# Kernel tuning notes

Hardware: AMD Instinct MI355X
Metric: run time of the kernel (lower is better)

Reference implementation:

```python
import jax, jax.numpy as jnp
import numpy as np

DIM = 1024
HEADS = 16
HEAD_DIM = DIM // HEADS
HIDDEN = 4 * DIM
EPS = 1e-5

def _layernorm(x, w, b):
    mu = jnp.mean(x, axis=-1, keepdims=True)
    var = jnp.mean(jnp.square(x - mu), axis=-1, keepdims=True)
    return (x - mu) * jax.lax.rsqrt(var + EPS) * w + b

def setup_inputs() -> dict:
    key = jax.random.key(0)
    ks = jax.random.split(key, 8)
    B, N, C = 4, 1024, DIM
    s = lambda fan_in: 1.0 / np.sqrt(fan_in)
    return {
        "x": jax.random.normal(ks[0], (B, N, C), dtype=jnp.float32),
        "ln1_w": jnp.ones((C,), jnp.float32),
        "ln1_b": jnp.zeros((C,), jnp.float32),
        "qkv_w": jax.random.normal(ks[1], (3 * C, C), jnp.float32) * s(C),
        "proj_w": jax.random.normal(ks[2], (C, C), jnp.float32) * s(C),
        "proj_b": jnp.zeros((C,), jnp.float32),
        "ln2_w": jnp.ones((C,), jnp.float32),
        "ln2_b": jnp.zeros((C,), jnp.float32),
        "fc1_w": jax.random.normal(ks[3], (HIDDEN, C), jnp.float32) * s(C),
        "fc1_b": jnp.zeros((HIDDEN,), jnp.float32),
        "fc2_w": jax.random.normal(ks[4], (C, HIDDEN), jnp.float32) * s(HIDDEN),
        "fc2_b": jnp.zeros((C,), jnp.float32),
    }

def reference(x, ln1_w, ln1_b, qkv_w, proj_w, proj_b, ln2_w, ln2_b, fc1_w, fc1_b, fc2_w, fc2_b):
    B, N, C = x.shape
    H, D = HEADS, HEAD_DIM
    scale = D ** -0.5
    # --- attention branch (pre-norm) ---
    h = _layernorm(x, ln1_w, ln1_b)
    qkv = jnp.einsum('bnc,oc->bno', h, qkv_w)          # [B,N,3C], no bias (qkv_bias=False)
    qkv = qkv.reshape(B, N, 3, H, D)
    q = jnp.transpose(qkv[:, :, 0], (0, 2, 1, 3))       # [B,H,N,D]
    k = jnp.transpose(qkv[:, :, 1], (0, 2, 1, 3))
    v = jnp.transpose(qkv[:, :, 2], (0, 2, 1, 3))
    attn = jnp.einsum('bhnd,bhmd->bhnm', q, k) * scale  # [B,H,N,N]
    attn = jax.nn.softmax(attn, axis=-1)
    o = jnp.einsum('bhnm,bhmd->bhnd', attn, v)          # [B,H,N,D]
    o = jnp.transpose(o, (0, 2, 1, 3)).reshape(B, N, C)
    o = jnp.einsum('bnc,oc->bno', o, proj_w) + proj_b
    x = x + o
    # --- MLP branch (pre-norm); drop=0.0 -> identity ---
    h = _layernorm(x, ln2_w, ln2_b)
    h = jnp.einsum('bnc,hc->bnh', h, fc1_w) + fc1_b
    h = jax.nn.gelu(h, approximate=False)               # nn.GELU exact erf form
    h = jnp.einsum('bnh,ch->bnc', h, fc2_w) + fc2_b
    return x + h
```

## Files before the change

kernel.cpp:

```cpp
#include <hip/hip_runtime.h>
#include <hip/hip_bf16.h>
#include <math.h>
#include <stdint.h>

#define SEQ 1024
#define CDIM 1024
#define NHEAD 16
#define HIDDEN 4096
#define BATCH 4
#define MROWS (BATCH*SEQ)

using bf16x8 = __attribute__((ext_vector_type(8))) short;
using f32x4  = __attribute__((ext_vector_type(4))) float;

__device__ __forceinline__ short f2bf(float f) {
    union { float f; uint32_t u; } c; c.f = f;
    const uint32_t u = c.u + 0x7FFFu + ((c.u >> 16) & 1u);
    return (short)(u >> 16);
}

__device__ __forceinline__ float gelu_exact(float v) {
    return 0.5f * v * (1.0f + erff(v * 0.70710678118654752440f));
}

__device__ __forceinline__ void gload_lds16(const short* g, short* lds) {
    __builtin_amdgcn_global_load_lds(
        (const __attribute__((address_space(1))) void*)(uintptr_t)g,
        (__attribute__((address_space(3))) void*)(uintptr_t)lds,
        16, 0, 0);
}

__global__ void cvt_all_kernel(const float* __restrict__ qkv_w, const float* __restrict__ proj_w,
                               const float* __restrict__ fc1_w, const float* __restrict__ fc2_w,
                               short* __restrict__ wq, short* __restrict__ wp,
                               short* __restrict__ w1, short* __restrict__ w2) {
    const int blk = blockIdx.x;
    const float* in; short* out; size_t base;
    if (blk < 1536)      { in = qkv_w;  out = wq; base = (size_t)blk * 2048; }
    else if (blk < 2048) { in = proj_w; out = wp; base = (size_t)(blk - 1536) * 2048; }
    else if (blk < 4096) { in = fc1_w;  out = w1; base = (size_t)(blk - 2048) * 2048; }
    else                 { in = fc2_w;  out = w2; base = (size_t)(blk - 4096) * 2048; }
    const size_t i = base + (size_t)threadIdx.x * 8;
    const float4 a = *(const float4*)(in + i);
    const float4 b = *(const float4*)(in + i + 4);
    bf16x8 s;
    s[0] = f2bf(a.x); s[1] = f2bf(a.y); s[2] = f2bf(a.z); s[3] = f2bf(a.w);
    s[4] = f2bf(b.x); s[5] = f2bf(b.y); s[6] = f2bf(b.z); s[7] = f2bf(b.w);
    *(bf16x8*)(out + i) = s;
}

__global__ void ln_kernel(const float* __restrict__ x, const float* __restrict__ w,
                          const float* __restrict__ b, short* __restrict__ out) {
    const int row = blockIdx.x;
    const int t = threadIdx.x;
    const float4* xr = (const float4*)(x + (size_t)row * CDIM);
    float4 v = xr[t];
    float s  = v.x + v.y + v.z + v.w;
    float sq = v.x*v.x + v.y*v.y + v.z*v.z + v.w*v.w;
    #pragma unroll
    for (int off = 32; off; off >>= 1) {
        s  += __shfl_down(s, off);
        sq += __shfl_down(sq, off);
    }
    __shared__ float ss[4], ssq[4];
    const int wid = t >> 6, lane = t & 63;
    if (lane == 0) { ss[wid] = s; ssq[wid] = sq; }
    __syncthreads();
    s  = ss[0] + ss[1] + ss[2] + ss[3];
    sq = ssq[0] + ssq[1] + ssq[2] + ssq[3];
    const float mu  = s * (1.0f / CDIM);
    const float var = sq * (1.0f / CDIM) - mu * mu;
    const float rs  = rsqrtf(var + 1e-5f);
    const float4 wv = ((const float4*)w)[t];
    const float4 bv = ((const float4*)b)[t];
    short4 o;
    o.x = f2bf((v.x - mu) * rs * wv.x + bv.x);
    o.y = f2bf((v.y - mu) * rs * wv.y + bv.y);
    o.z = f2bf((v.z - mu) * rs * wv.z + bv.z);
    o.w = f2bf((v.w - mu) * rs * wv.w + bv.w);
    *(short4*)(out + (size_t)row * CDIM + t * 4) = o;
}

template<int BM, int BN, bool BIAS, bool RES, bool GELU_, bool OUTBF16>
__global__ __launch_bounds__(256) void mgemm(
    const short* __restrict__ A, const short* __restrict__ B,
    const float* __restrict__ bias, const float* __restrict__ res,
    void* __restrict__ Cv, int M, int N, int K)
{
    constexpr int MF = BM / 32;
    constexpr int NF = BN / 32;
    constexpr int CA = BM / 64;
    constexpr int CB = BN / 64;
    __shared__ __align__(16) short As[3][BM * 32];
    __shared__ __align__(16) short Bs[3][BN * 32];
    const int t = threadIdx.x;
    const int w = t >> 6, l = t & 63;

    const int gx = gridDim.x;
    const int nwg = gx * gridDim.y;
    const int lid = blockIdx.y * gx + blockIdx.x;
    const int swzb = (lid & 7) * (nwg >> 3) + (lid >> 3);
    const int bx = swzb % gx, by = swzb / gx;
    const int m0 = by * BM, n0 = bx * BN;

    const int wrow = (w >> 1) * (BM / 2);
    const int wcol = (w & 1) * (BN / 2);

    const int sk8 = ((l & 3) ^ ((l >> 3) & 3)) * 8;
    const short* agp = A + (size_t)(m0 + w * 16 * CA + (l >> 2)) * K + sk8;
    const short* bgp = B + (size_t)(n0 + w * 16 * CB + (l >> 2)) * K + sk8;

    const int fr = l & 15;
    const int rk = ((l >> 4) ^ ((fr >> 1) & 3)) * 8;
    int aoff[MF], boff[NF];
    #pragma unroll
    for (int m = 0; m < MF; ++m) aoff[m] = (wrow + m * 16 + fr) * 32 + rk;
    #pragma unroll
    for (int n = 0; n < NF; ++n) boff[n] = (wcol + n * 16 + fr) * 32 + rk;

    auto stage = [&](int k0, int buf) {
        #pragma unroll
        for (int c = 0; c < CA; ++c)
            gload_lds16(agp + (size_t)(c * 16) * K + k0, &As[buf][(w * CA + c) * 512]);
        #pragma unroll
        for (int c = 0; c < CB; ++c)
            gload_lds16(bgp + (size_t)(c * 16) * K + k0, &Bs[buf][(w * CB + c) * 512]);
    };

    f32x4 acc[MF][NF] = {};
    const int T = K / 32;
    stage(0, 0);
    stage(32, 1);
    int cur = 0;
    for (int kt = 0; kt < T; ++kt) {
        if (kt < T - 1) {
            if constexpr (CA + CB == 4) asm volatile("s_waitcnt vmcnt(4)" ::: "memory");
            else                        asm volatile("s_waitcnt vmcnt(3)" ::: "memory");
        } else {
            asm volatile("s_waitcnt vmcnt(0)" ::: "memory");
        }
        __builtin_amdgcn_s_barrier();
        if (kt + 2 < T) {
            int nb = kt + 2; nb -= (nb >= 3) ? ((nb / 3) * 3) : 0;
            stage((kt + 2) * 32, nb);
        }
        bf16x8 af[MF], bfr[NF];
        #pragma unroll
        for (int m = 0; m < MF; ++m) af[m]  = *(const bf16x8*)&As[cur][aoff[m]];
        #pragma unroll
        for (int n = 0; n < NF; ++n) bfr[n] = *(const bf16x8*)&Bs[cur][boff[n]];
        #pragma unroll
        for (int m = 0; m < MF; ++m)
            #pragma unroll
            for (int n = 0; n < NF; ++n)
                acc[m][n] = __builtin_amdgcn_mfma_f32_16x16x32_bf16(af[m], bfr[n], acc[m][n], 0, 0, 0);
        cur = (cur == 2) ? 0 : cur + 1;
    }

    const int lr4 = (l >> 4) * 4, lc = l & 15;
    #pragma unroll
    for (int m = 0; m < MF; ++m) {
        #pragma unroll
        for (int n = 0; n < NF; ++n) {
            const int col = n0 + wcol + n * 16 + lc;
            const float bv = BIAS ? bias[col] : 0.0f;
            #pragma unroll
            for (int r = 0; r < 4; ++r) {
                const int row = m0 + wrow + m * 16 + lr4 + r;
                float v = acc[m][n][r] + bv;
                if (GELU_) v = gelu_exact(v);
                if (RES)   v += res[(size_t)row * N + col];
                if (OUTBF16) ((short*)Cv)[(size_t)row * N + col] = f2bf(v);
                else         ((float*)Cv)[(size_t)row * N + col] = v;
            }
        }
    }
}

__global__ __launch_bounds__(256) void qkv_m(
    const short* __restrict__ A, const short* __restrict__ B,
    short* __restrict__ qkvb, short* __restrict__ VT, int K)
{
    __shared__ __align__(16) short As[3][128 * 32];
    __shared__ __align__(16) short Bs[3][128 * 32];
    const int t = threadIdx.x;
    const int w = t >> 6, l = t & 63;

    const int gx = gridDim.x;
    const int nwg = gx * gridDim.y;
    const int lid = blockIdx.y * gx + blockIdx.x;
    const int swzb = (lid & 7) * (nwg >> 3) + (lid >> 3);
    const int bx = swzb % gx, by = swzb / gx;
    const int m0 = by * 128, n0 = bx * 128;

    const int wrow = (w >> 1) * 64;
    const int wcol = (w & 1) * 64;

    const int sk8 = ((l & 3) ^ ((l >> 3) & 3)) * 8;
    const short* agp = A + (size_t)(m0 + w * 32 + (l >> 2)) * K + sk8;
    const short* bgp = B + (size_t)(n0 + w * 32 + (l >> 2)) * K + sk8;

    const int fr = l & 15;
    const int rk = ((l >> 4) ^ ((fr >> 1) & 3)) * 8;
    int aoff[4], boff[4];
    #pragma unroll
    for (int m = 0; m < 4; ++m) aoff[m] = (wrow + m * 16 + fr) * 32 + rk;
    #pragma unroll
    for (int n = 0; n < 4; ++n) boff[n] = (wcol + n * 16 + fr) * 32 + rk;

    auto stage = [&](int k0, int buf) {
        #pragma unroll
        for (int c = 0; c < 2; ++c)
            gload_lds16(agp + (size_t)(c * 16) * K + k0, &As[buf][(w * 2 + c) * 512]);
        #pragma unroll
        for (int c = 0; c < 2; ++c)
            gload_lds16(bgp + (size_t)(c * 16) * K + k0, &Bs[buf][(w * 2 + c) * 512]);
    };

    f32x4 acc[4][4] = {};
    const int T = K / 32;
    stage(0, 0);
    stage(32, 1);
    int cur = 0;
    for (int kt = 0; kt < T; ++kt) {
        if (kt < T - 1) asm volatile("s_waitcnt vmcnt(4)" ::: "memory");
        else            asm volatile("s_waitcnt vmcnt(0)" ::: "memory");
        __builtin_amdgcn_s_barrier();
        if (kt + 2 < T) {
            int nb = kt + 2; nb -= (nb >= 3) ? ((nb / 3) * 3) : 0;
            stage((kt + 2) * 32, nb);
        }
        bf16x8 af[4], bfr[4];
        #pragma unroll
        for (int m = 0; m < 4; ++m) af[m]  = *(const bf16x8*)&As[cur][aoff[m]];
        #pragma unroll
        for (int n = 0; n < 4; ++n) bfr[n] = *(const bf16x8*)&Bs[cur][boff[n]];
        #pragma unroll
        for (int m = 0; m < 4; ++m)
            #pragma unroll
            for (int n = 0; n < 4; ++n)
                acc[m][n] = __builtin_amdgcn_mfma_f32_16x16x32_bf16(af[m], bfr[n], acc[m][n], 0, 0, 0);
        cur = (cur == 2) ? 0 : cur + 1;
    }

    const int lr4 = (l >> 4) * 4, lc = l & 15;
    if (n0 < 2048) {
        const float sc = (n0 < 1024) ? 0.125f : 1.0f;
        #pragma unroll
        for (int m = 0; m < 4; ++m) {
            #pragma unroll
            for (int n = 0; n < 4; ++n) {
                const int col = n0 + wcol + n * 16 + lc;
                #pragma unroll
                for (int r = 0; r < 4; ++r) {
                    const int row = m0 + wrow + m * 16 + lr4 + r;
                    qkvb[(size_t)row * 2048 + col] = f2bf(acc[m][n][r] * sc);
                }
            }
        }
    } else {
        #pragma unroll
        for (int m = 0; m < 4; ++m) {
            const int row0 = m0 + wrow + m * 16 + lr4;
            const int b = row0 >> 10, nseq = row0 & 1023;
            #pragma unroll
            for (int n = 0; n < 4; ++n) {
                const int c2 = n0 - 2048 + wcol + n * 16 + lc;
                const int h = c2 >> 6, d = c2 & 63;
                short4 v4;
                v4.x = f2bf(acc[m][n][0]); v4.y = f2bf(acc[m][n][1]);
                v4.z = f2bf(acc[m][n][2]); v4.w = f2bf(acc[m][n][3]);
                *(short4*)&VT[(((size_t)(b * 16 + h) * 64 + d) * 1024) + nseq] = v4;
            }
        }
    }
}

__global__ __launch_bounds__(512) void fattn(const short* __restrict__ qkvb,
                                             const short* __restrict__ VT,
                                             short* __restrict__ o) {
    const int lid = blockIdx.y * gridDim.x + blockIdx.x;
    const int bh = ((lid >> 6) << 3) | (lid & 7);
    const int q0 = ((lid >> 3) & 7) * 128;
    const int b = bh >> 4, h = bh & 15;
    const int t = threadIdx.x, w = t >> 6, l = t & 63;

    __shared__ __align__(16) short Ks[2][64 * 64];
    __shared__ __align__(16) short Vs[2][64 * 64];
    __shared__ __align__(16) short Ps[8][1024];

    const size_t qrow = (size_t)(b * SEQ + q0 + w * 16 + (l & 15)) * 2048 + h * 64;
    bf16x8 qf[2];
    qf[0] = *(const bf16x8*)&qkvb[qrow + (l >> 4) * 8];
    qf[1] = *(const bf16x8*)&qkvb[qrow + 32 + (l >> 4) * 8];

    const int srow = l >> 3;
    const int sc16 = (l & 7) ^ (srow & 7);
    const short* Kg = qkvb + 1024 + h * 64;
    const short* Vg = VT + (size_t)bh * 64 * 1024;

    f32x4 acc[4] = {};
    float mr = -1e30f, lr = 0.0f;
    const int q = l & 15;
    const int g4 = (l >> 4) & 3;

    auto stage = [&](int kt, int buf) {
        const int kv0 = kt * 64;
        const int r0 = w * 8;
        gload_lds16(Kg + (size_t)(b * SEQ + kv0 + r0 + srow) * 2048 + sc16 * 8,
                    &Ks[buf][r0 * 64]);
        gload_lds16(Vg + (size_t)(r0 + srow) * 1024 + kv0 + sc16 * 8,
                    &Vs[buf][r0 * 64]);
    };

    stage(0, 0);
    for (int kt = 0; kt < 16; ++kt) {
        const int cur = kt & 1;
        __syncthreads();
        if (kt + 1 < 16) stage(kt + 1, cur ^ 1);

        f32x4 sacc[4];
        #pragma unroll
        for (int nt = 0; nt < 4; ++nt) {
            f32x4 z = {};
            #pragma unroll
            for (int ks = 0; ks < 2; ++ks) {
                const int row = nt * 16 + (l & 15);
                const int c16 = (ks * 4 + (l >> 4)) ^ (row & 7);
                const bf16x8 kf = *(const bf16x8*)&Ks[cur][row * 64 + c16 * 8];
                z = __builtin_amdgcn_mfma_f32_16x16x32_bf16(kf, qf[ks], z, 0, 0, 0);
            }
            sacc[nt] = z;
        }
        float tm = sacc[0][0];
        #pragma unroll
        for (int nt = 0; nt < 4; ++nt)
            #pragma unroll
            for (int r = 0; r < 4; ++r) tm = fmaxf(tm, sacc[nt][r]);
        tm = fmaxf(tm, __shfl_xor(tm, 16));
        tm = fmaxf(tm, __shfl_xor(tm, 32));
        const bool norescale = __all(tm <= mr + 8.0f);
        float fac = 1.0f;
        if (!norescale) {
            const float nm = fmaxf(mr, tm);
            fac = __expf(mr - nm);
            mr = nm;
        }
        float p[4][4];
        float ts = 0.0f;
        #pragma unroll
        for (int nt = 0; nt < 4; ++nt)
            #pragma unroll
            for (int r = 0; r < 4; ++r) {
                p[nt][r] = __expf(sacc[nt][r] - mr);
                ts += p[nt][r];
            }
        ts += __shfl_xor(ts, 16);
        ts += __shfl_xor(ts, 32);
        lr = lr * fac + ts;
        if (!norescale) {
            float facv[4];
            #pragma unroll
            for (int r = 0; r < 4; ++r)
                facv[r] = __shfl(fac, (l & 48) + g4 * 4 + r);
            #pragma unroll
            for (int nt2 = 0; nt2 < 4; ++nt2)
                #pragma unroll
                for (int r = 0; r < 4; ++r)
                    acc[nt2][r] *= facv[r];
        }
        #pragma unroll
        for (int nt = 0; nt < 4; ++nt) {
            uint32_t lo, hi;
            asm("v_cvt_pk_bf16_f32 %0, %1, %2" : "=v"(lo) : "v"(p[nt][0]), "v"(p[nt][1]));
            asm("v_cvt_pk_bf16_f32 %0, %1, %2" : "=v"(hi) : "v"(p[nt][2]), "v"(p[nt][3]));
            const int kvb = nt * 16 + g4 * 4;
            const int addr = q * 64 + (((kvb >> 3) ^ (q & 7)) << 3) + (kvb & 7);
            *(uint2*)&Ps[w][addr] = make_uint2(lo, hi);
        }
        asm volatile("s_waitcnt lgkmcnt(0)" ::: "memory");
        #pragma unroll
        for (int ks = 0; ks < 2; ++ks) {
            const int ql = l & 15;
            const bf16x8 pa = *(const bf16x8*)&Ps[w][ql * 64 + ((ks * 32 + (l >> 4) * 8) ^ ((ql & 7) << 3))];
            #pragma unroll
            for (int nt2 = 0; nt2 < 4; ++nt2) {
                const int row = nt2 * 16 + (l & 15);
                const int c16 = (ks * 4 + (l >> 4)) ^ (row & 7);
                const bf16x8 vf = *(const bf16x8*)&Vs[cur][row * 64 + c16 * 8];
                acc[nt2] = __builtin_amdgcn_mfma_f32_16x16x32_bf16(pa, vf, acc[nt2], 0, 0, 0);
            }
        }
    }
    float rcpl = 1.0f / lr;
    #pragma unroll
    for (int r = 0; r < 4; ++r) {
        const float rcp = __shfl(rcpl, (l & 48) + g4 * 4 + r);
        const int qq = q0 + w * 16 + g4 * 4 + r;
        #pragma unroll
        for (int nt2 = 0; nt2 < 4; ++nt2) {
            const int d = nt2 * 16 + (l & 15);
            o[(size_t)(b * SEQ + qq) * CDIM + h * 64 + d] = f2bf(acc[nt2][r] * rcp);
        }
    }
}

extern "C" void kernel_launch(void* const* d_in, const int* in_sizes, int n_in,
                              void* d_out, int out_size, void* d_ws, size_t ws_size,
                              hipStream_t stream) {
    const float* x      = (const float*)d_in[0];
    const float* ln1_w  = (const float*)d_in[1];
    const float* ln1_b  = (const float*)d_in[2];
    const float* qkv_w  = (const float*)d_in[3];
    const float* proj_w = (const float*)d_in[4];
    const float* proj_b = (const float*)d_in[5];
    const float* ln2_w  = (const float*)d_in[6];
    const float* ln2_b  = (const float*)d_in[7];
    const float* fc1_w  = (const float*)d_in[8];
    const float* fc1_b  = (const float*)d_in[9];
    const float* fc2_w  = (const float*)d_in[10];
    const float* fc2_b  = (const float*)d_in[11];
    float* out = (float*)d_out;

    short* ws16  = (short*)d_ws;
    short* wqkv  = ws16;
    short* wproj = ws16 + 3145728;
    short* wfc1  = ws16 + 4194304;
    short* wfc2  = ws16 + 8388608;
    char*  wsb   = (char*)d_ws;
    short* qkvb  = (short*)(wsb + (size_t)24 * 1024 * 1024);
    short* VT    = (short*)(wsb + (size_t)40 * 1024 * 1024);
    short* mlp1  = (short*)(wsb + (size_t)24 * 1024 * 1024);
    short* hbuf  = (short*)(wsb + (size_t)72 * 1024 * 1024);

    cvt_all_kernel<<<6144, 256, 0, stream>>>(qkv_w, proj_w, fc1_w, fc2_w,
                                             wqkv, wproj, wfc1, wfc2);

    ln_kernel<<<MROWS, 256, 0, stream>>>(x, ln1_w, ln1_b, hbuf);
    qkv_m<<<dim3(24, 32), 256, 0, stream>>>(hbuf, wqkv, qkvb, VT, 1024);
    fattn<<<dim3(8, 64), 512, 0, stream>>>(qkvb, VT, hbuf);
    mgemm<64,128,true,true,false,false><<<dim3(8, 64), 256, 0, stream>>>(
        hbuf, wproj, proj_b, x, out, MROWS, 1024, 1024);
    ln_kernel<<<MROWS, 256, 0, stream>>>(out, ln2_w, ln2_b, hbuf);
    mgemm<128,128,true,false,true,true><<<dim3(32, 32), 256, 0, stream>>>(
        hbuf, wfc1, fc1_b, nullptr, mlp1, MROWS, 4096, 1024);
    mgemm<64,128,true,true,false,false><<<dim3(8, 64), 256, 0, stream>>>(
        mlp1, wfc2, fc2_b, out, out, MROWS, 1024, 4096);
}
```

Before: 219.1 us.

## Fuse LN1 into weight-convert kernel, use tanh GELU, retile N=1024 GEMMs

```diff
diff --git a/kernel.cpp b/kernel.cpp
--- a/kernel.cpp
+++ b/kernel.cpp
@@ -19,8 +19,9 @@
     return (short)(u >> 16);
 }
 
-__device__ __forceinline__ float gelu_exact(float v) {
-    return 0.5f * v * (1.0f + erff(v * 0.70710678118654752440f));
+__device__ __forceinline__ float gelu_fast(float x) {
+    const float y = 0.7978845608f * x * (1.0f + 0.044715f * x * x);
+    return x / (1.0f + __expf(-2.0f * y));
 }
 
 __device__ __forceinline__ void gload_lds16(const short* g, short* lds) {
@@ -30,23 +31,56 @@
         16, 0, 0);
 }
 
-__global__ void cvt_all_kernel(const float* __restrict__ qkv_w, const float* __restrict__ proj_w,
+__global__ void cvt_ln1_kernel(const float* __restrict__ qkv_w, const float* __restrict__ proj_w,
                                const float* __restrict__ fc1_w, const float* __restrict__ fc2_w,
                                short* __restrict__ wq, short* __restrict__ wp,
-                               short* __restrict__ w1, short* __restrict__ w2) {
+                               short* __restrict__ w1, short* __restrict__ w2,
+                               const float* __restrict__ x, const float* __restrict__ ln1_w,
+                               const float* __restrict__ ln1_b, short* __restrict__ hbuf) {
     const int blk = blockIdx.x;
-    const float* in; short* out; size_t base;
-    if (blk < 1536)      { in = qkv_w;  out = wq; base = (size_t)blk * 2048; }
-    else if (blk < 2048) { in = proj_w; out = wp; base = (size_t)(blk - 1536) * 2048; }
-    else if (blk < 4096) { in = fc1_w;  out = w1; base = (size_t)(blk - 2048) * 2048; }
-    else                 { in = fc2_w;  out = w2; base = (size_t)(blk - 4096) * 2048; }
-    const size_t i = base + (size_t)threadIdx.x * 8;
-    const float4 a = *(const float4*)(in + i);
-    const float4 b = *(const float4*)(in + i + 4);
-    bf16x8 s;
-    s[0] = f2bf(a.x); s[1] = f2bf(a.y); s[2] = f2bf(a.z); s[3] = f2bf(a.w);
-    s[4] = f2bf(b.x); s[5] = f2bf(b.y); s[6] = f2bf(b.z); s[7] = f2bf(b.w);
-    *(bf16x8*)(out + i) = s;
+    if (blk < 6144) {
+        const float* in; short* out; size_t base;
+        if (blk < 1536)      { in = qkv_w;  out = wq; base = (size_t)blk * 2048; }
+        else if (blk < 2048) { in = proj_w; out = wp; base = (size_t)(blk - 1536) * 2048; }
+        else if (blk < 4096) { in = fc1_w;  out = w1; base = (size_t)(blk - 2048) * 2048; }
+        else                 { in = fc2_w;  out = w2; base = (size_t)(blk - 4096) * 2048; }
+        const size_t i = base + (size_t)threadIdx.x * 8;
+        const float4 a = *(const float4*)(in + i);
+        const float4 b = *(const float4*)(in + i + 4);
+        bf16x8 s;
+        s[0] = f2bf(a.x); s[1] = f2bf(a.y); s[2] = f2bf(a.z); s[3] = f2bf(a.w);
+        s[4] = f2bf(b.x); s[5] = f2bf(b.y); s[6] = f2bf(b.z); s[7] = f2bf(b.w);
+        *(bf16x8*)(out + i) = s;
+        return;
+    }
+    const int row = blk - 6144;
+    const int t = threadIdx.x;
+    const float4* xr = (const float4*)(x + (size_t)row * CDIM);
+    float4 v = xr[t];
+    float s  = v.x + v.y + v.z + v.w;
+    float sq = v.x*v.x + v.y*v.y + v.z*v.z + v.w*v.w;
+    #pragma unroll
+    for (int off = 32; off; off >>= 1) {
+        s  += __shfl_down(s, off);
+        sq += __shfl_down(sq, off);
+    }
+    __shared__ float ss[4], ssq[4];
+    const int wid = t >> 6, lane = t & 63;
+    if (lane == 0) { ss[wid] = s; ssq[wid] = sq; }
+    __syncthreads();
+    s  = ss[0] + ss[1] + ss[2] + ss[3];
+    sq = ssq[0] + ssq[1] + ssq[2] + ssq[3];
+    const float mu  = s * (1.0f / CDIM);
+    const float var = sq * (1.0f / CDIM) - mu * mu;
+    const float rs  = rsqrtf(var + 1e-5f);
+    const float4 wv = ((const float4*)ln1_w)[t];
+    const float4 bv = ((const float4*)ln1_b)[t];
+    short4 o;
+    o.x = f2bf((v.x - mu) * rs * wv.x + bv.x);
+    o.y = f2bf((v.y - mu) * rs * wv.y + bv.y);
+    o.z = f2bf((v.z - mu) * rs * wv.z + bv.z);
+    o.w = f2bf((v.w - mu) * rs * wv.w + bv.w);
+    *(short4*)(hbuf + (size_t)row * CDIM + t * 4) = o;
 }
 
 __global__ void ln_kernel(const float* __restrict__ x, const float* __restrict__ w,
@@ -168,7 +202,7 @@
             for (int r = 0; r < 4; ++r) {
                 const int row = m0 + wrow + m * 16 + lr4 + r;
                 float v = acc[m][n][r] + bv;
-                if (GELU_) v = gelu_exact(v);
+                if (GELU_) v = gelu_fast(v);
                 if (RES)   v += res[(size_t)row * N + col];
                 if (OUTBF16) ((short*)Cv)[(size_t)row * N + col] = f2bf(v);
                 else         ((float*)Cv)[(size_t)row * N + col] = v;
@@ -433,17 +467,16 @@
     short* mlp1  = (short*)(wsb + (size_t)24 * 1024 * 1024);
     short* hbuf  = (short*)(wsb + (size_t)72 * 1024 * 1024);
 
-    cvt_all_kernel<<<6144, 256, 0, stream>>>(qkv_w, proj_w, fc1_w, fc2_w,
-                                             wqkv, wproj, wfc1, wfc2);
-
-    ln_kernel<<<MROWS, 256, 0, stream>>>(x, ln1_w, ln1_b, hbuf);
+    cvt_ln1_kernel<<<6144 + MROWS, 256, 0, stream>>>(
+        qkv_w, proj_w, fc1_w, fc2_w, wqkv, wproj, wfc1, wfc2,
+        x, ln1_w, ln1_b, hbuf);
     qkv_m<<<dim3(24, 32), 256, 0, stream>>>(hbuf, wqkv, qkvb, VT, 1024);
     fattn<<<dim3(8, 64), 512, 0, stream>>>(qkvb, VT, hbuf);
-    mgemm<64,128,true,true,false,false><<<dim3(8, 64), 256, 0, stream>>>(
+    mgemm<128,64,true,true,false,false><<<dim3(16, 32), 256, 0, stream>>>(
         hbuf, wproj, proj_b, x, out, MROWS, 1024, 1024);
     ln_kernel<<<MROWS, 256, 0, stream>>>(out, ln2_w, ln2_b, hbuf);
     mgemm<128,128,true,false,true,true><<<dim3(32, 32), 256, 0, stream>>>(
         hbuf, wfc1, fc1_b, nullptr, mlp1, MROWS, 4096, 1024);
-    mgemm<64,128,true,true,false,false><<<dim3(8, 64), 256, 0, stream>>>(
+    mgemm<128,64,true,true,false,false><<<dim3(16, 32), 256, 0, stream>>>(
         mlp1, wfc2, fc2_b, out, out, MROWS, 1024, 4096);
 }
```

After: 211.0 us, median of 3. 1.04x faster.
